# Optimization experiments

Measured on AMD Instinct MI355X. Metric: run time of the kernel, lower is better.

Reference implementation:

```python
import jax, jax.numpy as jnp
import numpy as np

N_RAYS = 8192
N_SAMPLES = 128
HIDDEN = 128
SH_DIM = 16
RAY_EXT_FACTOR = 10.0


def rsh_cart_3(d):
    # Real spherical harmonics up to degree 3, Cartesian form (16 coeffs).
    x, y, z = d[..., 0], d[..., 1], d[..., 2]
    x2, y2, z2 = x * x, y * y, z * z
    xy, yz, xz = x * y, y * z, x * z
    return jnp.stack([
        0.282094791773878 * jnp.ones_like(x),
        -0.48860251190292 * y,
        0.48860251190292 * z,
        -0.48860251190292 * x,
        1.0925484305920792 * xy,
        -1.0925484305920792 * yz,
        0.94617469575756 * z2 - 0.31539156525252,
        -1.0925484305920792 * xz,
        0.5462742152960396 * (x2 - y2),
        0.5900435899266435 * y * (-3.0 * x2 + y2),
        2.8906114426405538 * xy * z,
        0.4570457994644658 * y * (1.0 - 5.0 * z2),
        0.3731763325901154 * z * (5.0 * z2 - 3.0),
        0.4570457994644658 * x * (1.0 - 5.0 * z2),
        1.445305721320277 * z * (x2 - y2),
        0.5900435899266435 * x * (-x2 + 3.0 * y2),
    ], axis=-1)


def setup_inputs() -> dict:
    key = jax.random.key(0)
    ks = jax.random.split(key, 11)
    o = jax.random.normal(ks[0], (N_RAYS, 3), dtype=jnp.float32)
    origins = 2.5 * o / jnp.linalg.norm(o, axis=-1, keepdims=True)
    # aim roughly at the unit AABB so most rays are active
    dirs = -origins + 0.2 * jax.random.normal(ks[1], (N_RAYS, 3), dtype=jnp.float32)
    u = jax.random.uniform(ks[2], (N_RAYS, N_SAMPLES), dtype=jnp.float32)
    s1 = 1.0 / np.sqrt(3.0)
    s2 = 1.0 / np.sqrt(HIDDEN)
    s3 = 1.0 / np.sqrt(HIDDEN + SH_DIM)
    return {
        'origins': origins,
        'dirs': dirs,
        'u': u,
        'W1': s1 * jax.random.normal(ks[3], (3, HIDDEN), dtype=jnp.float32),
        'b1': jnp.zeros((HIDDEN,), jnp.float32),
        'W2': s2 * jax.random.normal(ks[4], (HIDDEN, HIDDEN), dtype=jnp.float32),
        'b2': jnp.zeros((HIDDEN,), jnp.float32),
        'Wd': s2 * jax.random.normal(ks[5], (HIDDEN, 1), dtype=jnp.float32),
        'bd': jnp.zeros((1,), jnp.float32),
        'Wc': s3 * jax.random.normal(ks[6], (HIDDEN + SH_DIM, 3), dtype=jnp.float32),
        'bc': jnp.zeros((3,), jnp.float32),
    }


def reference(origins, dirs, u, W1, b1, W2, b2, Wd, bd, Wc, bc):
    B, T = u.shape
    # ---- AABB ([-1,1]^3) slab intersection -> tnear/tfar, active mask ----
    inv_d = 1.0 / dirs
    t1 = (-1.0 - origins) * inv_d
    t2 = (1.0 - origins) * inv_d
    tnear = jnp.maximum(jnp.max(jnp.minimum(t1, t2), axis=-1), 0.0)  # (B,)
    tfar = jnp.min(jnp.maximum(t1, t2), axis=-1)                      # (B,)
    active = tfar > tnear                                             # (B,)
    tfar_c = jnp.maximum(tfar, tnear + 1e-3)
    # ---- stratified ray step sampling ----
    frac = (jnp.arange(T, dtype=u.dtype) + u) / T                     # (B,T)
    ts = tnear[:, None] + (tfar_c - tnear)[:, None] * frac            # (B,T)
    xyz = origins[:, None, :] + dirs[:, None, :] * ts[..., None]      # (B,T,3)
    # aabb is [-1,1]^3 so ndc == xyz; spatial filter = bounds test
    xyz_ndc = xyz
    mask = jnp.all(jnp.abs(xyz_ndc) <= 1.0, axis=-1) & active[:, None]  # (B,T)
    dnorm = jnp.linalg.norm(dirs, axis=-1)                            # (B,)
    ynm = rsh_cart_3(dirs / dnorm[:, None])                           # (B,16)
    # ---- radiance field MLP over all sample points ----
    x = xyz_ndc.reshape(B * T, 3)
    h = jax.nn.relu(x @ W1 + b1)
    h = jax.nn.relu(h @ W2 + b2)
    sigma = jax.nn.softplus(h @ Wd + bd).reshape(B, T)
    cond = jnp.broadcast_to(ynm[:, None, :], (B, T, SH_DIM)).reshape(B * T, SH_DIM)
    color = jax.nn.sigmoid(jnp.concatenate([h, cond], axis=-1) @ Wc + bc).reshape(B, T, 3)
    # zero out points rejected by the spatial filter (torch writes only masked)
    sigma = sigma * mask
    color = color * mask[..., None]
    # ---- transmittance integration (integrate_timesteps) ----
    tfinal = tfar_c * RAY_EXT_FACTOR
    deltas = jnp.diff(ts, axis=-1, append=tfinal[:, None])            # (B,T)
    sd = sigma * deltas * dnorm[:, None]
    csum = jnp.cumsum(sd, axis=-1)
    # weights_i = T_i * alpha_i = exp(-csum_{i-1}) - exp(-csum_i)
    weights = jnp.exp(sd - csum) - jnp.exp(-csum)                     # (B,T)
    color_out = jnp.einsum('bt,btc->bc', weights, color)              # (B,3)
    alpha_out = jnp.sum(weights, axis=-1, keepdims=True)              # (B,1)
    rgba = jnp.concatenate([color_out, alpha_out], axis=-1)           # (B,4)
    return jnp.where(active[:, None], rgba, 0.0)
```

## Files before the change

kernel.cpp:

```cpp
#include <hip/hip_runtime.h>
#include <math.h>

#define NRAYS 8192
#define T 128
#define H 128
#define SHD 16

using short8 = __attribute__((ext_vector_type(8))) short;
using f32x4  = __attribute__((ext_vector_type(4))) float;
using f32x2  = __attribute__((ext_vector_type(2))) float;
using u32x2  = __attribute__((ext_vector_type(2))) unsigned;

__device__ __forceinline__ float fexp(float x) {
  return exp2f(x * 1.44269504088896341f);
}
__device__ __forceinline__ float softplus_f(float x) {
  return fmaxf(x, 0.f) + 0.693147180559945309f * log2f(1.f + fexp(-fabsf(x)));
}
__device__ __forceinline__ float sigmoid_f(float x) {
  return __builtin_amdgcn_rcpf(1.f + fexp(-x));
}

__device__ __forceinline__ unsigned f2bf(float f) {
  unsigned u = __float_as_uint(f);
  return (u + 0x7fffu + ((u >> 16) & 1u)) >> 16;
}

__device__ __forceinline__ unsigned pk2(f32x2 h) {
  unsigned r;
  asm("v_cvt_pk_bf16_f32 %0, %1, %2" : "=v"(r) : "v"(h[0]), "v"(h[1]));
  return r;
}

__global__ void preprocess(const float* __restrict__ W2, const float* __restrict__ Wd,
                           const float* __restrict__ Wc, const float* __restrict__ bc,
                           const float* __restrict__ origins, const float* __restrict__ dirs,
                           unsigned short* __restrict__ w2t,
                           unsigned short* __restrict__ woutf,
                           float* __restrict__ rayp_all) {
  const int t = blockIdx.x * 256 + threadIdx.x;
  if (t < 16384) {
    const int n = t >> 7, p = t & 127;
    const int o = (p >> 3) ^ (n & 7);
    const int k = o * 8 + (p & 7);
    w2t[t] = (unsigned short)f2bf(W2[k * 128 + n]);
  }
  if (t < 2048) {
    const int kk = t >> 9, L = (t >> 3) & 63, j = t & 7;
    const int c = L & 15, g = L >> 4;
    const int k = kk * 32 + g * 8 + j;
    float v = 0.f;
    if (c == 0) v = Wd[k];
    else if (c < 4) v = Wc[k * 3 + (c - 1)];
    woutf[t] = (unsigned short)f2bf(v);
  }
  if (t < NRAYS) {
    const float ox = origins[t*3+0], oy = origins[t*3+1], oz = origins[t*3+2];
    const float dx = dirs[t*3+0],  dy = dirs[t*3+1],  dz = dirs[t*3+2];
    const float ix = 1.f/dx, iy = 1.f/dy, iz = 1.f/dz;
    const float t1x = (-1.f-ox)*ix, t2x = (1.f-ox)*ix;
    const float t1y = (-1.f-oy)*iy, t2y = (1.f-oy)*iy;
    const float t1z = (-1.f-oz)*iz, t2z = (1.f-oz)*iz;
    float tnear = fmaxf(fmaxf(fminf(t1x,t2x), fminf(t1y,t2y)), fminf(t1z,t2z));
    tnear = fmaxf(tnear, 0.f);
    const float tfar = fminf(fminf(fmaxf(t1x,t2x), fmaxf(t1y,t2y)), fmaxf(t1z,t2z));
    const bool  active = tfar > tnear;
    const float tfar_c = fmaxf(tfar, tnear + 1e-3f);
    const float dnorm = sqrtf(dx*dx + dy*dy + dz*dz);
    const float nx = dx/dnorm, ny = dy/dnorm, nz = dz/dnorm;
    const float x2 = nx*nx, y2 = ny*ny, z2 = nz*nz;
    const float xy = nx*ny, yz = ny*nz, xz = nx*nz;
    float ynm[16];
    ynm[0]  = 0.282094791773878f;
    ynm[1]  = -0.48860251190292f*ny;
    ynm[2]  = 0.48860251190292f*nz;
    ynm[3]  = -0.48860251190292f*nx;
    ynm[4]  = 1.0925484305920792f*xy;
    ynm[5]  = -1.0925484305920792f*yz;
    ynm[6]  = 0.94617469575756f*z2 - 0.31539156525252f;
    ynm[7]  = -1.0925484305920792f*xz;
    ynm[8]  = 0.5462742152960396f*(x2-y2);
    ynm[9]  = 0.5900435899266435f*ny*(-3.f*x2+y2);
    ynm[10] = 2.8906114426405538f*xy*nz;
    ynm[11] = 0.4570457994644658f*ny*(1.f-5.f*z2);
    ynm[12] = 0.3731763325901154f*nz*(5.f*z2-3.f);
    ynm[13] = 0.4570457994644658f*nx*(1.f-5.f*z2);
    ynm[14] = 1.445305721320277f*nz*(x2-y2);
    ynm[15] = 0.5900435899266435f*nx*(-x2+3.f*y2);
    float cp0 = bc[0], cp1 = bc[1], cp2 = bc[2];
    #pragma unroll
    for (int s = 0; s < SHD; ++s) {
      cp0 = fmaf(ynm[s], Wc[(H+s)*3+0], cp0);
      cp1 = fmaf(ynm[s], Wc[(H+s)*3+1], cp1);
      cp2 = fmaf(ynm[s], Wc[(H+s)*3+2], cp2);
    }
    rayp_all[t*8+0] = tfar_c;
    rayp_all[t*8+1] = dnorm;
    rayp_all[t*8+2] = active ? 1.f : 0.f;
    rayp_all[t*8+3] = cp0;
    rayp_all[t*8+4] = cp1;
    rayp_all[t*8+5] = cp2;
    rayp_all[t*8+6] = tnear;
    rayp_all[t*8+7] = 0.f;
  }
}

__global__ __launch_bounds__(256, 4) void nerf_render(
    const float* __restrict__ origins, const float* __restrict__ dirs,
    const float* __restrict__ u, const float* __restrict__ W1,
    const float* __restrict__ b1, const float* __restrict__ b2,
    const float* __restrict__ bd, const unsigned short* __restrict__ w2t,
    const unsigned short* __restrict__ woutf, const float* __restrict__ rayp_all,
    float* __restrict__ out)
{
  const int ray = blockIdx.x;
  const int tid = threadIdx.x;
  const int L = tid & 63;
  const int w = tid >> 6;
  const int g = L >> 4;
  const int c = L & 15;

  __shared__ __align__(16) short Bs[16384];
  __shared__ __align__(16) float baseA[H];
  __shared__ __align__(16) float slopeA[H];
  __shared__ float ts_s[T];
  __shared__ float mask_s[T];
  __shared__ float wred[2][4];
  __shared__ float wtot[2];

  const float tfar_c = rayp_all[ray*8+0];
  const float dnorm  = rayp_all[ray*8+1];
  const float actf   = rayp_all[ray*8+2];
  const float cpo0   = rayp_all[ray*8+3];
  const float cpo1   = rayp_all[ray*8+4];
  const float cpo2   = rayp_all[ray*8+5];
  const float tnear  = rayp_all[ray*8+6];

  {
    const float4* src = (const float4*)w2t;
    float4* dst = (float4*)Bs;
    #pragma unroll
    for (int i = 0; i < 8; ++i) dst[tid + i * 256] = src[tid + i * 256];
  }

  if (tid < T) {
    const int tl = tid;
    const float ox = origins[ray*3+0], oy = origins[ray*3+1], oz = origins[ray*3+2];
    const float dx = dirs[ray*3+0],  dy = dirs[ray*3+1],  dz = dirs[ray*3+2];
    const bool active = actf != 0.f;
    const float ut = u[ray*T + tl];
    const float frac = ((float)tl + ut) * (1.f/(float)T);
    const float tt = tnear + (tfar_c - tnear) * frac;
    const float px = fmaf(dx, tt, ox);
    const float py = fmaf(dy, tt, oy);
    const float pz = fmaf(dz, tt, oz);
    ts_s[tl] = tt;
    const bool m = (fabsf(px) <= 1.f) && (fabsf(py) <= 1.f) && (fabsf(pz) <= 1.f) && active;
    mask_s[tl] = m ? 1.f : 0.f;
    const float w0 = W1[tl], w1v = W1[H + tl], w2v = W1[2*H + tl];
    baseA[tl]  = fmaf(ox, w0, fmaf(oy, w1v, fmaf(oz, w2v, b1[tl])));
    slopeA[tl] = fmaf(dx, w0, fmaf(dy, w1v, dz * w2v));
  }

  f32x4 acc[2][8];
  #pragma unroll
  for (int mt = 0; mt < 8; ++mt) {
    const float4 bv = *(const float4*)&b2[mt*16 + g*4];
    #pragma unroll
    for (int tm = 0; tm < 2; ++tm) {
      acc[tm][mt][0] = bv.x; acc[tm][mt][1] = bv.y;
      acc[tm][mt][2] = bv.z; acc[tm][mt][3] = bv.w;
    }
  }
  __syncthreads();

  const float t0 = ts_s[32*w + c];
  const float t1 = ts_s[32*w + 16 + c];
  const f32x2 tz0 = {t0, t0}, tz1 = {t1, t1};
  const f32x2 zero2 = {0.f, 0.f};

  #pragma unroll
  for (int ks = 0; ks < 4; ++ks) {
    const int kb = ks*32 + g*8;
    const f32x4 bq0 = *(const f32x4*)&baseA[kb];
    const f32x4 bq1 = *(const f32x4*)&baseA[kb+4];
    const f32x4 sq0 = *(const f32x4*)&slopeA[kb];
    const f32x4 sq1 = *(const f32x4*)&slopeA[kb+4];
    const f32x2 b01 = {bq0[0], bq0[1]}, b23 = {bq0[2], bq0[3]};
    const f32x2 b45 = {bq1[0], bq1[1]}, b67 = {bq1[2], bq1[3]};
    const f32x2 s01 = {sq0[0], sq0[1]}, s23 = {sq0[2], sq0[3]};
    const f32x2 s45 = {sq1[0], sq1[1]}, s67 = {sq1[2], sq1[3]};
    const f32x2 a01 = __builtin_elementwise_max(__builtin_elementwise_fma(tz0, s01, b01), zero2);
    const f32x2 a23 = __builtin_elementwise_max(__builtin_elementwise_fma(tz0, s23, b23), zero2);
    const f32x2 a45 = __builtin_elementwise_max(__builtin_elementwise_fma(tz0, s45, b45), zero2);
    const f32x2 a67 = __builtin_elementwise_max(__builtin_elementwise_fma(tz0, s67, b67), zero2);
    const f32x2 e01 = __builtin_elementwise_max(__builtin_elementwise_fma(tz1, s01, b01), zero2);
    const f32x2 e23 = __builtin_elementwise_max(__builtin_elementwise_fma(tz1, s23, b23), zero2);
    const f32x2 e45 = __builtin_elementwise_max(__builtin_elementwise_fma(tz1, s45, b45), zero2);
    const f32x2 e67 = __builtin_elementwise_max(__builtin_elementwise_fma(tz1, s67, b67), zero2);
    union U { uint4 u; short8 s; } A0, A1;
    A0.u = make_uint4(pk2(a01), pk2(a23), pk2(a45), pk2(a67));
    A1.u = make_uint4(pk2(e01), pk2(e23), pk2(e45), pk2(e67));
    const int swb = ((ks*4 + g) ^ (c & 7)) * 8;
    #pragma unroll
    for (int mt = 0; mt < 8; ++mt) {
      const short8 wf = *(const short8*)&Bs[(mt*16 + c)*128 + swb];
      acc[0][mt] = __builtin_amdgcn_mfma_f32_16x16x32_bf16(wf, A0.s, acc[0][mt], 0, 0, 0);
      acc[1][mt] = __builtin_amdgcn_mfma_f32_16x16x32_bf16(wf, A1.s, acc[1][mt], 0, 0, 0);
    }
  }
  __syncthreads();
  float4* SredP = (float4*)Bs;
  short*  As2   = Bs + 2048;

  short* As2w = As2 + w * 640;
  short8 wa[4];
  #pragma unroll
  for (int kk = 0; kk < 4; ++kk)
    wa[kk] = *(const short8*)&woutf[(kk*64 + L)*8];

  #pragma unroll
  for (int tm = 0; tm < 2; ++tm) {
    f32x4 oacc;
    oacc[0] = 0.f; oacc[1] = 0.f; oacc[2] = 0.f; oacc[3] = 0.f;
    #pragma unroll
    for (int kk = 0; kk < 4; ++kk) {
      #pragma unroll
      for (int i = 0; i < 2; ++i) {
        const f32x4 a = acc[tm][kk*2 + i];
        const f32x2 h01 = __builtin_elementwise_max((f32x2){a[0], a[1]}, zero2);
        const f32x2 h23 = __builtin_elementwise_max((f32x2){a[2], a[3]}, zero2);
        *(uint2*)&As2w[c*40 + i*16 + g*4] = make_uint2(pk2(h01), pk2(h23));
      }
      const short8 hbf = *(const short8*)&As2w[c*40 + g*8];
      oacc = __builtin_amdgcn_mfma_f32_16x16x32_bf16(wa[kk], hbf, oacc, 0, 0, 0);
    }
    if (g == 0)
      SredP[32*w + 16*tm + c] = make_float4(oacc[0], oacc[1], oacc[2], oacc[3]);
  }
  __syncthreads();

  float sd = 0.f, cc0 = 0.f, cc1 = 0.f, cc2 = 0.f;
  if (tid < T) {
    const float4 sv = SredP[tid];
    const float mk = mask_s[tid];
    const float sigma = softplus_f(sv.x + bd[0]) * mk;
    cc0 = mk * sigmoid_f(sv.y + cpo0);
    cc1 = mk * sigmoid_f(sv.z + cpo1);
    cc2 = mk * sigmoid_f(sv.w + cpo2);
    const float tt = ts_s[tid];
    const float tnext = (tid < T-1) ? ts_s[tid + 1] : tfar_c * 10.f;
    sd = sigma * (tnext - tt) * dnorm;
  }

  float val = sd;
  #pragma unroll
  for (int off = 1; off < 64; off <<= 1) {
    const float tmp = __shfl_up(val, off);
    if (L >= off) val += tmp;
  }
  if (tid < T && L == 63) wtot[w] = val;
  __syncthreads();
  const float csum = val + ((w == 1) ? wtot[0] : 0.f);

  float wgt = 0.f, wcx = 0.f, wcy = 0.f, wcz = 0.f;
  if (tid < T) {
    wgt = fexp(sd - csum) - fexp(-csum);
    wcx = wgt * cc0; wcy = wgt * cc1; wcz = wgt * cc2;
  }
  #pragma unroll
  for (int mm = 32; mm >= 1; mm >>= 1) {
    wgt += __shfl_xor(wgt, mm);
    wcx += __shfl_xor(wcx, mm);
    wcy += __shfl_xor(wcy, mm);
    wcz += __shfl_xor(wcz, mm);
  }
  if (tid < T && L == 0) {
    wred[w][0] = wgt; wred[w][1] = wcx; wred[w][2] = wcy; wred[w][3] = wcz;
  }
  __syncthreads();
  if (tid == 0) {
    const float aw = wred[0][0] + wred[1][0];
    const float o0 = wred[0][1] + wred[1][1];
    const float o1 = wred[0][2] + wred[1][2];
    const float o2 = wred[0][3] + wred[1][3];
    const bool act = actf != 0.f;
    out[ray*4+0] = act ? o0 : 0.f;
    out[ray*4+1] = act ? o1 : 0.f;
    out[ray*4+2] = act ? o2 : 0.f;
    out[ray*4+3] = act ? aw : 0.f;
  }
}

extern "C" void kernel_launch(void* const* d_in, const int* in_sizes, int n_in,
                              void* d_out, int out_size, void* d_ws, size_t ws_size,
                              hipStream_t stream) {
  const float* origins = (const float*)d_in[0];
  const float* dirs    = (const float*)d_in[1];
  const float* u       = (const float*)d_in[2];
  const float* W1      = (const float*)d_in[3];
  const float* b1      = (const float*)d_in[4];
  const float* W2      = (const float*)d_in[5];
  const float* b2      = (const float*)d_in[6];
  const float* Wd      = (const float*)d_in[7];
  const float* bd      = (const float*)d_in[8];
  const float* Wc      = (const float*)d_in[9];
  const float* bc      = (const float*)d_in[10];

  unsigned short* w2t      = (unsigned short*)d_ws;
  unsigned short* woutf    = (unsigned short*)((char*)d_ws + 32768);
  float*          rayp_all = (float*)((char*)d_ws + 36864);

  preprocess<<<64, 256, 0, stream>>>(W2, Wd, Wc, bc, origins, dirs,
                                     w2t, woutf, rayp_all);
  nerf_render<<<NRAYS, 256, 0, stream>>>(origins, dirs, u, W1, b1, b2, bd,
                                         w2t, woutf, rayp_all, (float*)d_out);
}
```

Before: 133.2 us.

## Process eight rays per block to reuse staged W2 and streamline the scan epilogue

Each block now loops over eight rays, so the 32 KB bf16 W2 tile is copied from global memory into LDS once per eight rays instead of once per ray, and the grid shrinks eightfold. The epilogue no longer round-trips MFMA outputs through shared memory: every wave computes sigma and colours in registers, runs a 16-lane DPP prefix scan, and combines per-wave totals through a small shared array. This also lets all four waves take part in integration and removes one barrier per ray. In exchange, ray iterations inside a block run serially, with fewer blocks available to hide latency.

Result: slower. 167.0 us (+25.3%).

```diff
diff --git a/kernel.cpp b/kernel.cpp
--- a/kernel.cpp
+++ b/kernel.cpp
@@ -9,7 +9,6 @@
 using short8 = __attribute__((ext_vector_type(8))) short;
 using f32x4  = __attribute__((ext_vector_type(4))) float;
 using f32x2  = __attribute__((ext_vector_type(2))) float;
-using u32x2  = __attribute__((ext_vector_type(2))) unsigned;
 
 __device__ __forceinline__ float fexp(float x) {
   return exp2f(x * 1.44269504088896341f);
@@ -30,6 +29,24 @@
   unsigned r;
   asm("v_cvt_pk_bf16_f32 %0, %1, %2" : "=v"(r) : "v"(h[0]), "v"(h[1]));
   return r;
+}
+
+template<int N>
+__device__ __forceinline__ float dpp_shr0(float v) {
+  return __builtin_bit_cast(float,
+    __builtin_amdgcn_update_dpp(0, __builtin_bit_cast(int, v),
+                                0x110 | N, 0xf, 0xf, false));
+}
+__device__ __forceinline__ float scan16(float v) {
+  v += dpp_shr0<1>(v);
+  v += dpp_shr0<2>(v);
+  v += dpp_shr0<4>(v);
+  v += dpp_shr0<8>(v);
+  return v;
+}
+__device__ __forceinline__ float readlane15f(float v) {
+  return __builtin_bit_cast(float,
+    __builtin_amdgcn_readlane(__builtin_bit_cast(int, v), 15));
 }
 
 __global__ void preprocess(const float* __restrict__ W2, const float* __restrict__ Wd,
@@ -113,7 +130,6 @@
     const unsigned short* __restrict__ woutf, const float* __restrict__ rayp_all,
     float* __restrict__ out)
 {
-  const int ray = blockIdx.x;
   const int tid = threadIdx.x;
   const int L = tid & 63;
   const int w = tid >> 6;
@@ -121,20 +137,13 @@
   const int c = L & 15;
 
   __shared__ __align__(16) short Bs[16384];
+  __shared__ __align__(16) short As2[4 * 640];
   __shared__ __align__(16) float baseA[H];
   __shared__ __align__(16) float slopeA[H];
-  __shared__ float ts_s[T];
-  __shared__ float mask_s[T];
-  __shared__ float wred[2][4];
-  __shared__ float wtot[2];
-
-  const float tfar_c = rayp_all[ray*8+0];
-  const float dnorm  = rayp_all[ray*8+1];
-  const float actf   = rayp_all[ray*8+2];
-  const float cpo0   = rayp_all[ray*8+3];
-  const float cpo1   = rayp_all[ray*8+4];
-  const float cpo2   = rayp_all[ray*8+5];
-  const float tnear  = rayp_all[ray*8+6];
+  __shared__ __align__(16) float ts_s[T];
+  __shared__ __align__(16) float mask_s[T];
+  __shared__ float wtot[4];
+  __shared__ float wred[4][4];
 
   {
     const float4* src = (const float4*)w2t;
@@ -143,152 +152,162 @@
     for (int i = 0; i < 8; ++i) dst[tid + i * 256] = src[tid + i * 256];
   }
 
-  if (tid < T) {
-    const int tl = tid;
-    const float ox = origins[ray*3+0], oy = origins[ray*3+1], oz = origins[ray*3+2];
-    const float dx = dirs[ray*3+0],  dy = dirs[ray*3+1],  dz = dirs[ray*3+2];
-    const bool active = actf != 0.f;
-    const float ut = u[ray*T + tl];
-    const float frac = ((float)tl + ut) * (1.f/(float)T);
-    const float tt = tnear + (tfar_c - tnear) * frac;
-    const float px = fmaf(dx, tt, ox);
-    const float py = fmaf(dy, tt, oy);
-    const float pz = fmaf(dz, tt, oz);
-    ts_s[tl] = tt;
-    const bool m = (fabsf(px) <= 1.f) && (fabsf(py) <= 1.f) && (fabsf(pz) <= 1.f) && active;
-    mask_s[tl] = m ? 1.f : 0.f;
-    const float w0 = W1[tl], w1v = W1[H + tl], w2v = W1[2*H + tl];
-    baseA[tl]  = fmaf(ox, w0, fmaf(oy, w1v, fmaf(oz, w2v, b1[tl])));
-    slopeA[tl] = fmaf(dx, w0, fmaf(dy, w1v, dz * w2v));
-  }
-
-  f32x4 acc[2][8];
-  #pragma unroll
-  for (int mt = 0; mt < 8; ++mt) {
-    const float4 bv = *(const float4*)&b2[mt*16 + g*4];
-    #pragma unroll
-    for (int tm = 0; tm < 2; ++tm) {
-      acc[tm][mt][0] = bv.x; acc[tm][mt][1] = bv.y;
-      acc[tm][mt][2] = bv.z; acc[tm][mt][3] = bv.w;
-    }
-  }
-  __syncthreads();
-
-  const float t0 = ts_s[32*w + c];
-  const float t1 = ts_s[32*w + 16 + c];
-  const f32x2 tz0 = {t0, t0}, tz1 = {t1, t1};
-  const f32x2 zero2 = {0.f, 0.f};
-
-  #pragma unroll
-  for (int ks = 0; ks < 4; ++ks) {
-    const int kb = ks*32 + g*8;
-    const f32x4 bq0 = *(const f32x4*)&baseA[kb];
-    const f32x4 bq1 = *(const f32x4*)&baseA[kb+4];
-    const f32x4 sq0 = *(const f32x4*)&slopeA[kb];
-    const f32x4 sq1 = *(const f32x4*)&slopeA[kb+4];
-    const f32x2 b01 = {bq0[0], bq0[1]}, b23 = {bq0[2], bq0[3]};
-    const f32x2 b45 = {bq1[0], bq1[1]}, b67 = {bq1[2], bq1[3]};
-    const f32x2 s01 = {sq0[0], sq0[1]}, s23 = {sq0[2], sq0[3]};
-    const f32x2 s45 = {sq1[0], sq1[1]}, s67 = {sq1[2], sq1[3]};
-    const f32x2 a01 = __builtin_elementwise_max(__builtin_elementwise_fma(tz0, s01, b01), zero2);
-    const f32x2 a23 = __builtin_elementwise_max(__builtin_elementwise_fma(tz0, s23, b23), zero2);
-    const f32x2 a45 = __builtin_elementwise_max(__builtin_elementwise_fma(tz0, s45, b45), zero2);
-    const f32x2 a67 = __builtin_elementwise_max(__builtin_elementwise_fma(tz0, s67, b67), zero2);
-    const f32x2 e01 = __builtin_elementwise_max(__builtin_elementwise_fma(tz1, s01, b01), zero2);
-    const f32x2 e23 = __builtin_elementwise_max(__builtin_elementwise_fma(tz1, s23, b23), zero2);
-    const f32x2 e45 = __builtin_elementwise_max(__builtin_elementwise_fma(tz1, s45, b45), zero2);
-    const f32x2 e67 = __builtin_elementwise_max(__builtin_elementwise_fma(tz1, s67, b67), zero2);
-    union U { uint4 u; short8 s; } A0, A1;
-    A0.u = make_uint4(pk2(a01), pk2(a23), pk2(a45), pk2(a67));
-    A1.u = make_uint4(pk2(e01), pk2(e23), pk2(e45), pk2(e67));
-    const int swb = ((ks*4 + g) ^ (c & 7)) * 8;
-    #pragma unroll
-    for (int mt = 0; mt < 8; ++mt) {
-      const short8 wf = *(const short8*)&Bs[(mt*16 + c)*128 + swb];
-      acc[0][mt] = __builtin_amdgcn_mfma_f32_16x16x32_bf16(wf, A0.s, acc[0][mt], 0, 0, 0);
-      acc[1][mt] = __builtin_amdgcn_mfma_f32_16x16x32_bf16(wf, A1.s, acc[1][mt], 0, 0, 0);
-    }
-  }
-  __syncthreads();
-  float4* SredP = (float4*)Bs;
-  short*  As2   = Bs + 2048;
-
-  short* As2w = As2 + w * 640;
   short8 wa[4];
   #pragma unroll
   for (int kk = 0; kk < 4; ++kk)
     wa[kk] = *(const short8*)&woutf[(kk*64 + L)*8];
 
-  #pragma unroll
-  for (int tm = 0; tm < 2; ++tm) {
-    f32x4 oacc;
-    oacc[0] = 0.f; oacc[1] = 0.f; oacc[2] = 0.f; oacc[3] = 0.f;
-    #pragma unroll
-    for (int kk = 0; kk < 4; ++kk) {
+  short* As2w = As2 + w * 640;
+  const f32x2 zero2 = {0.f, 0.f};
+  const float bd0 = bd[0];
+
+  #pragma unroll 1
+  for (int r = 0; r < 8; ++r) {
+    const int ray = blockIdx.x * 8 + r;
+    const float tfar_c = rayp_all[ray*8+0];
+    const float dnorm  = rayp_all[ray*8+1];
+    const float actf   = rayp_all[ray*8+2];
+    const float cpo0   = rayp_all[ray*8+3];
+    const float cpo1   = rayp_all[ray*8+4];
+    const float cpo2   = rayp_all[ray*8+5];
+    const float tnear  = rayp_all[ray*8+6];
+
+    if (tid < T) {
+      const int tl = tid;
+      const float ox = origins[ray*3+0], oy = origins[ray*3+1], oz = origins[ray*3+2];
+      const float dx = dirs[ray*3+0],  dy = dirs[ray*3+1],  dz = dirs[ray*3+2];
+      const bool active = actf != 0.f;
+      const float ut = u[ray*T + tl];
+      const float frac = ((float)tl + ut) * (1.f/(float)T);
+      const float tt = tnear + (tfar_c - tnear) * frac;
+      const float px = fmaf(dx, tt, ox);
+      const float py = fmaf(dy, tt, oy);
+      const float pz = fmaf(dz, tt, oz);
+      ts_s[tl] = tt;
+      const bool m = (fabsf(px) <= 1.f) && (fabsf(py) <= 1.f) && (fabsf(pz) <= 1.f) && active;
+      mask_s[tl] = m ? 1.f : 0.f;
+      const float w0v = W1[tl], w1v = W1[H + tl], w2v = W1[2*H + tl];
+      baseA[tl]  = fmaf(ox, w0v, fmaf(oy, w1v, fmaf(oz, w2v, b1[tl])));
+      slopeA[tl] = fmaf(dx, w0v, fmaf(dy, w1v, dz * w2v));
+    }
+
+    f32x4 acc[2][8];
+    #pragma unroll
+    for (int mt = 0; mt < 8; ++mt) {
+      const float4 bv = *(const float4*)&b2[mt*16 + g*4];
       #pragma unroll
-      for (int i = 0; i < 2; ++i) {
-        const f32x4 a = acc[tm][kk*2 + i];
-        const f32x2 h01 = __builtin_elementwise_max((f32x2){a[0], a[1]}, zero2);
-        const f32x2 h23 = __builtin_elementwise_max((f32x2){a[2], a[3]}, zero2);
-        *(uint2*)&As2w[c*40 + i*16 + g*4] = make_uint2(pk2(h01), pk2(h23));
+      for (int tm = 0; tm < 2; ++tm) {
+        acc[tm][mt][0] = bv.x; acc[tm][mt][1] = bv.y;
+        acc[tm][mt][2] = bv.z; acc[tm][mt][3] = bv.w;
       }
-      const short8 hbf = *(const short8*)&As2w[c*40 + g*8];
-      oacc = __builtin_amdgcn_mfma_f32_16x16x32_bf16(wa[kk], hbf, oacc, 0, 0, 0);
-    }
-    if (g == 0)
-      SredP[32*w + 16*tm + c] = make_float4(oacc[0], oacc[1], oacc[2], oacc[3]);
-  }
-  __syncthreads();
-
-  float sd = 0.f, cc0 = 0.f, cc1 = 0.f, cc2 = 0.f;
-  if (tid < T) {
-    const float4 sv = SredP[tid];
-    const float mk = mask_s[tid];
-    const float sigma = softplus_f(sv.x + bd[0]) * mk;
-    cc0 = mk * sigmoid_f(sv.y + cpo0);
-    cc1 = mk * sigmoid_f(sv.z + cpo1);
-    cc2 = mk * sigmoid_f(sv.w + cpo2);
-    const float tt = ts_s[tid];
-    const float tnext = (tid < T-1) ? ts_s[tid + 1] : tfar_c * 10.f;
-    sd = sigma * (tnext - tt) * dnorm;
-  }
-
-  float val = sd;
-  #pragma unroll
-  for (int off = 1; off < 64; off <<= 1) {
-    const float tmp = __shfl_up(val, off);
-    if (L >= off) val += tmp;
-  }
-  if (tid < T && L == 63) wtot[w] = val;
-  __syncthreads();
-  const float csum = val + ((w == 1) ? wtot[0] : 0.f);
-
-  float wgt = 0.f, wcx = 0.f, wcy = 0.f, wcz = 0.f;
-  if (tid < T) {
-    wgt = fexp(sd - csum) - fexp(-csum);
-    wcx = wgt * cc0; wcy = wgt * cc1; wcz = wgt * cc2;
-  }
-  #pragma unroll
-  for (int mm = 32; mm >= 1; mm >>= 1) {
-    wgt += __shfl_xor(wgt, mm);
-    wcx += __shfl_xor(wcx, mm);
-    wcy += __shfl_xor(wcy, mm);
-    wcz += __shfl_xor(wcz, mm);
-  }
-  if (tid < T && L == 0) {
-    wred[w][0] = wgt; wred[w][1] = wcx; wred[w][2] = wcy; wred[w][3] = wcz;
-  }
-  __syncthreads();
-  if (tid == 0) {
-    const float aw = wred[0][0] + wred[1][0];
-    const float o0 = wred[0][1] + wred[1][1];
-    const float o1 = wred[0][2] + wred[1][2];
-    const float o2 = wred[0][3] + wred[1][3];
-    const bool act = actf != 0.f;
-    out[ray*4+0] = act ? o0 : 0.f;
-    out[ray*4+1] = act ? o1 : 0.f;
-    out[ray*4+2] = act ? o2 : 0.f;
-    out[ray*4+3] = act ? aw : 0.f;
+    }
+    __syncthreads();
+
+    const float t0 = ts_s[32*w + c];
+    const float t1 = ts_s[32*w + 16 + c];
+    const f32x2 tz0 = {t0, t0}, tz1 = {t1, t1};
+
+    #pragma unroll
+    for (int ks = 0; ks < 4; ++ks) {
+      const int kb = ks*32 + g*8;
+      const f32x4 bq0 = *(const f32x4*)&baseA[kb];
+      const f32x4 bq1 = *(const f32x4*)&baseA[kb+4];
+      const f32x4 sq0 = *(const f32x4*)&slopeA[kb];
+      const f32x4 sq1 = *(const f32x4*)&slopeA[kb+4];
+      const f32x2 b01 = {bq0[0], bq0[1]}, b23 = {bq0[2], bq0[3]};
+      const f32x2 b45 = {bq1[0], bq1[1]}, b67 = {bq1[2], bq1[3]};
+      const f32x2 s01 = {sq0[0], sq0[1]}, s23 = {sq0[2], sq0[3]};
+      const f32x2 s45 = {sq1[0], sq1[1]}, s67 = {sq1[2], sq1[3]};
+      const f32x2 a01 = __builtin_elementwise_max(__builtin_elementwise_fma(tz0, s01, b01), zero2);
+      const f32x2 a23 = __builtin_elementwise_max(__builtin_elementwise_fma(tz0, s23, b23), zero2);
+      const f32x2 a45 = __builtin_elementwise_max(__builtin_elementwise_fma(tz0, s45, b45), zero2);
+      const f32x2 a67 = __builtin_elementwise_max(__builtin_elementwise_fma(tz0, s67, b67), zero2);
+      const f32x2 e01 = __builtin_elementwise_max(__builtin_elementwise_fma(tz1, s01, b01), zero2);
+      const f32x2 e23 = __builtin_elementwise_max(__builtin_elementwise_fma(tz1, s23, b23), zero2);
+      const f32x2 e45 = __builtin_elementwise_max(__builtin_elementwise_fma(tz1, s45, b45), zero2);
+      const f32x2 e67 = __builtin_elementwise_max(__builtin_elementwise_fma(tz1, s67, b67), zero2);
+      union U { uint4 u; short8 s; } A0, A1;
+      A0.u = make_uint4(pk2(a01), pk2(a23), pk2(a45), pk2(a67));
+      A1.u = make_uint4(pk2(e01), pk2(e23), pk2(e45), pk2(e67));
+      const int swb = ((ks*4 + g) ^ (c & 7)) * 8;
+      #pragma unroll
+      for (int mt = 0; mt < 8; ++mt) {
+        const short8 wf = *(const short8*)&Bs[(mt*16 + c)*128 + swb];
+        acc[0][mt] = __builtin_amdgcn_mfma_f32_16x16x32_bf16(wf, A0.s, acc[0][mt], 0, 0, 0);
+        acc[1][mt] = __builtin_amdgcn_mfma_f32_16x16x32_bf16(wf, A1.s, acc[1][mt], 0, 0, 0);
+      }
+    }
+
+    f32x4 osig[2];
+    #pragma unroll
+    for (int tm = 0; tm < 2; ++tm) {
+      f32x4 oacc;
+      oacc[0] = 0.f; oacc[1] = 0.f; oacc[2] = 0.f; oacc[3] = 0.f;
+      #pragma unroll
+      for (int kk = 0; kk < 4; ++kk) {
+        #pragma unroll
+        for (int i = 0; i < 2; ++i) {
+          const f32x4 a = acc[tm][kk*2 + i];
+          const f32x2 h01 = __builtin_elementwise_max((f32x2){a[0], a[1]}, zero2);
+          const f32x2 h23 = __builtin_elementwise_max((f32x2){a[2], a[3]}, zero2);
+          *(uint2*)&As2w[c*40 + i*16 + g*4] = make_uint2(pk2(h01), pk2(h23));
+        }
+        const short8 hbf = *(const short8*)&As2w[c*40 + g*8];
+        oacc = __builtin_amdgcn_mfma_f32_16x16x32_bf16(wa[kk], hbf, oacc, 0, 0, 0);
+      }
+      osig[tm] = oacc;
+    }
+
+    const int s0 = 32*w + c, s1 = s0 + 16;
+    const float ts0 = ts_s[s0], tn0 = ts_s[s0 + 1];
+    const float ts1 = ts_s[s1];
+    const float tn1 = (s1 < T-1) ? ts_s[s1 + 1] : tfar_c * 10.f;
+    const float d0 = mask_s[s0] * (tn0 - ts0) * dnorm;
+    const float d1 = mask_s[s1] * (tn1 - ts1) * dnorm;
+    const float sd0 = softplus_f(osig[0][0] + bd0) * d0;
+    const float sd1 = softplus_f(osig[1][0] + bd0) * d1;
+    float p0 = scan16(sd0);
+    const float tot0 = readlane15f(p0);
+    float p1 = scan16(sd1);
+    const float tot1 = readlane15f(p1);
+    if (L == 0) wtot[w] = tot0 + tot1;
+    __syncthreads();
+    float pre = 0.f;
+    if (w > 0) pre += wtot[0];
+    if (w > 1) pre += wtot[1];
+    if (w > 2) pre += wtot[2];
+    const float cs0 = pre + p0;
+    const float cs1 = pre + tot0 + p1;
+    const float w0 = fexp(sd0 - cs0) - fexp(-cs0);
+    const float w1 = fexp(sd1 - cs1) - fexp(-cs1);
+    float pw  = w0 + w1;
+    float pxc = w0 * sigmoid_f(osig[0][1] + cpo0) + w1 * sigmoid_f(osig[1][1] + cpo0);
+    float pyc = w0 * sigmoid_f(osig[0][2] + cpo1) + w1 * sigmoid_f(osig[1][2] + cpo1);
+    float pzc = w0 * sigmoid_f(osig[0][3] + cpo2) + w1 * sigmoid_f(osig[1][3] + cpo2);
+    #pragma unroll
+    for (int off = 1; off < 16; off <<= 1) {
+      pw  += __shfl_xor(pw, off);
+      pxc += __shfl_xor(pxc, off);
+      pyc += __shfl_xor(pyc, off);
+      pzc += __shfl_xor(pzc, off);
+    }
+    if (L == 0) {
+      wred[w][0] = pw; wred[w][1] = pxc; wred[w][2] = pyc; wred[w][3] = pzc;
+    }
+    __syncthreads();
+    if (tid == 0) {
+      const float aw = wred[0][0] + wred[1][0] + wred[2][0] + wred[3][0];
+      const float o0 = wred[0][1] + wred[1][1] + wred[2][1] + wred[3][1];
+      const float o1 = wred[0][2] + wred[1][2] + wred[2][2] + wred[3][2];
+      const float o2 = wred[0][3] + wred[1][3] + wred[2][3] + wred[3][3];
+      const bool act = actf != 0.f;
+      float4 o;
+      o.x = act ? o0 : 0.f;
+      o.y = act ? o1 : 0.f;
+      o.z = act ? o2 : 0.f;
+      o.w = act ? aw : 0.f;
+      *(float4*)&out[ray*4] = o;
+    }
   }
 }
 
@@ -313,6 +332,6 @@
 
   preprocess<<<64, 256, 0, stream>>>(W2, Wd, Wc, bc, origins, dirs,
                                      w2t, woutf, rayp_all);
-  nerf_render<<<NRAYS, 256, 0, stream>>>(origins, dirs, u, W1, b1, b2, bd,
-                                         w2t, woutf, rayp_all, (float*)d_out);
-}
+  nerf_render<<<NRAYS/8, 256, 0, stream>>>(origins, dirs, u, W1, b1, b2, bd,
+                                           w2t, woutf, rayp_all, (float*)d_out);
+}
```
